# Performance work log

Measured on AMD Instinct MI355X. Metric: run time of the kernel, lower is better.

Reference implementation:

```python
import jax, jax.numpy as jnp
import numpy as np

T, B, D = 32, 16, 128


def _evolve(xr, xi, U):
    # xr, xi: [T,B,D,D]; U: [D,D,2] -> complex U x U^H per matrix
    Ur, Ui = U[..., 0], U[..., 1]
    r = jnp.einsum('ij,tbjk->tbik', Ur, xr) - jnp.einsum('ij,tbjk->tbik', Ui, xi)
    i = jnp.einsum('ij,tbjk->tbik', Ui, xr) + jnp.einsum('ij,tbjk->tbik', Ur, xi)
    out_r = jnp.einsum('tbik,jk->tbij', r, Ur) + jnp.einsum('tbik,jk->tbij', i, Ui)
    out_i = jnp.einsum('tbik,jk->tbij', i, Ur) - jnp.einsum('tbik,jk->tbij', r, Ui)
    return out_r, out_i


def _forward(inputs_real, inputs_imag, Uq, Uk, Uv):
    qr, qi = _evolve(inputs_real, inputs_imag, Uq)
    kr, ki = _evolve(inputs_real, inputs_imag, Uk)
    vr, vi = _evolve(inputs_real, inputs_imag, Uv)
    # trace(A @ B) = sum_ij A_ij * B_ji -> distance scores [Tq, Tk, B]
    tr_r = jnp.einsum('qbij,kbji->qkb', qr, kr) - jnp.einsum('qbij,kbji->qkb', qi, ki)
    tr_i = jnp.einsum('qbij,kbji->qkb', qr, ki) + jnp.einsum('qbij,kbji->qkb', qi, kr)
    dist = jnp.sqrt(tr_r * tr_r + tr_i * tr_i)
    # original builds scores via torch.tensor(list) -> values are detached
    dist = jax.lax.stop_gradient(dist)
    # original applies softmax over the LAST dim of the [Tk, B] score matrix,
    # i.e. over the batch dim (faithful reproduction)
    S = jax.nn.softmax(dist, axis=-1)  # [Tq, Tk, B]
    # original zip(values[0], values[1], scores) iterates the (real, imag)
    # components of the value at t=0 and t=1 against score rows 0 and 1
    s0 = S[:, 0, :, None, None]  # [Tq,B,1,1]
    s1 = S[:, 1, :, None, None]
    out_r = vr[0][None] * s0 + vi[0][None] * s1  # [Tq,B,D,D]
    out_i = vr[1][None] * s0 + vi[1][None] * s1
    return out_r, out_i


def setup_inputs() -> dict:
    key = jax.random.key(0)
    k0, k1, k2, k3, k4 = jax.random.split(key, 5)
    inputs_real = jax.random.normal(k0, (T, B, D, D), dtype=jnp.float32)
    inputs_imag = jax.random.normal(k1, (T, B, D, D), dtype=jnp.float32)
    eye = jnp.stack([jnp.eye(D, dtype=jnp.float32), jnp.zeros((D, D), jnp.float32)], axis=-1)
    Uq = eye + 0.05 * jax.random.normal(k2, (D, D, 2), dtype=jnp.float32)
    Uk = eye + 0.05 * jax.random.normal(k3, (D, D, 2), dtype=jnp.float32)
    Uv = eye + 0.05 * jax.random.normal(k4, (D, D, 2), dtype=jnp.float32)
    return {"inputs_real": inputs_real, "inputs_imag": inputs_imag, "Uq": Uq, "Uk": Uk, "Uv": Uv}


def reference(inputs_real, inputs_imag, Uq, Uk, Uv):
    return _forward(inputs_real, inputs_imag, Uq, Uk, Uv)
```

## Files before the change

### kernel.cpp

```cpp
#include <hip/hip_runtime.h>
#include <math.h>

#define MAT 16384
#define OFF_MC   0
#define OFF_MTC  32768
#define OFF_UVTC 65536
#define OFF_ZSR  2129920
#define OFF_ZSI  (OFF_ZSR + 32*16384)
#define OFF_VR   (OFF_ZSI + 32*16384)
#define OFF_VI   (OFF_VR + 32*16384)
#define OFF_TR   (OFF_VI + 32*16384)
#define OFF_S    (OFF_TR + 2048)

__device__ __forceinline__ float dot4(float4 a, float4 b) {
    return a.x*b.x + a.y*b.y + a.z*b.z + a.w*b.w;
}

__global__ __launch_bounds__(128) void k_M(const float* __restrict__ Uq,
                                           const float* __restrict__ Uk,
                                           const float* __restrict__ Uv,
                                           float* __restrict__ ws) {
    const int i = blockIdx.x;
    const int j = threadIdx.x;
    __shared__ float qr_s[128], qi_s[128];
    qr_s[j] = Uq[(j*128 + i)*2 + 0];
    qi_s[j] = Uq[(j*128 + i)*2 + 1];
    __syncthreads();
    const float2* Uk2 = (const float2*)Uk;
    float mr = 0.f, mi = 0.f;
    #pragma unroll 8
    for (int p = 0; p < 128; ++p) {
        float2 k2 = Uk2[p*128 + j];
        float qr = qr_s[p], qi = qi_s[p];
        mr += qr*k2.x + qi*k2.y;
        mi += qr*k2.y - qi*k2.x;
    }
    ws[OFF_MC  + i*256 + 2*j]     = mr;
    ws[OFF_MC  + i*256 + 2*j + 1] = mi;
    ws[OFF_MTC + j*256 + 2*i]     = mr;
    ws[OFF_MTC + j*256 + 2*i + 1] = mi;
    float2 uv = ((const float2*)Uv)[i*128 + j];
    ws[OFF_UVTC + j*256 + 2*i]     = uv.x;
    ws[OFF_UVTC + j*256 + 2*i + 1] = uv.y;
}

__global__ __launch_bounds__(128) void k_fused(const float* __restrict__ xr,
                                               const float* __restrict__ xi,
                                               const float* __restrict__ Uv,
                                               float* __restrict__ ws) {
    const int bid  = blockIdx.x;
    const int m    = bid & 63;
    const int i0   = (bid >> 6) * 8;
    const int tid  = threadIdx.x;
    const int w    = tid >> 6;
    const int lane = tid & 63;
    const int cg   = lane & 31;
    const int kp   = lane >> 5;

    __shared__ __align__(16) float At[2048];
    __shared__ __align__(16) float Tb[2112];

    {
        const float2* Ap2 = (const float2*)((m < 32) ? (ws + OFF_MC) : Uv);
        #pragma unroll
        for (int rr = 0; rr < 8; ++rr) {
            float2 u = Ap2[(i0 + rr)*128 + tid];
            *(float2*)&At[tid*16 + (rr>>2)*8 + (rr&3)*2] = u;
        }
    }
    __syncthreads();

    float yr[4][4], yi[4][4];
    #pragma unroll
    for (int r = 0; r < 4; ++r)
        #pragma unroll
        for (int c = 0; c < 4; ++c) { yr[r][c] = 0.f; yi[r][c] = 0.f; }

    const float4* Xr4 = (const float4*)(xr + (m & 31)*MAT);
    const float4* Xi4 = (const float4*)(xi + (m & 31)*MAT);

    float4 pR0, pI0, pR1, pI1;
#define LDX(T, R, I) do { int _k = 2*(T) + kp;               \
    R = Xr4[_k*32 + cg]; I = Xi4[_k*32 + cg]; } while (0)

#define CFMA_P1(aLo, aHi, Rv, Iv) do {                                   \
    const float ar_[4] = {aLo.x, aLo.z, aHi.x, aHi.z};                   \
    const float ai_[4] = {aLo.y, aLo.w, aHi.y, aHi.w};                   \
    const float br_[4] = {Rv.x, Rv.y, Rv.z, Rv.w};                       \
    const float bi_[4] = {Iv.x, Iv.y, Iv.z, Iv.w};                       \
    _Pragma("unroll")                                                    \
    for (int r = 0; r < 4; ++r) {                                        \
        _Pragma("unroll")                                                \
        for (int c = 0; c < 4; ++c) {                                    \
            yr[r][c] += ar_[r]*br_[c] - ai_[r]*bi_[c];                   \
            yi[r][c] += ar_[r]*bi_[c] + ai_[r]*br_[c];                   \
        }                                                                \
    } } while (0)

    LDX(0, pR0, pI0);
    LDX(1, pR1, pI1);
    #pragma unroll 1
    for (int t = 0; t < 64; t += 2) {
        {
            int kk = 2*t + kp;
            float4 aLo = *(const float4*)&At[kk*16 + w*8];
            float4 aHi = *(const float4*)&At[kk*16 + w*8 + 4];
            CFMA_P1(aLo, aHi, pR0, pI0);
            int tn = (t+2 > 63) ? 63 : t+2; LDX(tn, pR0, pI0);
        }
        {
            int kk = 2*(t+1) + kp;
            float4 aLo = *(const float4*)&At[kk*16 + w*8];
            float4 aHi = *(const float4*)&At[kk*16 + w*8 + 4];
            CFMA_P1(aLo, aHi, pR1, pI1);
            int tn = (t+3 > 63) ? 63 : t+3; LDX(tn, pR1, pI1);
        }
    }

    #pragma unroll
    for (int r = 0; r < 4; ++r)
        #pragma unroll
        for (int c = 0; c < 4; ++c) {
            yr[r][c] += __shfl_xor(yr[r][c], 32);
            yi[r][c] += __shfl_xor(yi[r][c], 32);
        }
    __syncthreads();
    if (kp == 0) {
        #pragma unroll
        for (int c = 0; c < 4; ++c) {
            int col = 4*cg + c;
            *(float4*)&At[col*16 + w*8]     = make_float4(yr[0][c], yi[0][c], yr[1][c], yi[1][c]);
            *(float4*)&At[col*16 + w*8 + 4] = make_float4(yr[2][c], yi[2][c], yr[3][c], yi[3][c]);
        }
    }
    __syncthreads();

    float zr[4][4], zi[4][4];
    #pragma unroll
    for (int r = 0; r < 4; ++r)
        #pragma unroll
        for (int c = 0; c < 4; ++c) { zr[r][c] = 0.f; zi[r][c] = 0.f; }

    const float4* UT4 = (const float4*)(ws + (m < 32 ? OFF_MTC : OFF_UVTC));

    float4 pE0, pO0, pE1, pO1;
#define LDU(T, E, O) do { int _k = 2*(T) + kp;               \
    E = UT4[_k*64 + 2*cg]; O = UT4[_k*64 + 2*cg + 1]; } while (0)

#define CFMA_P2(aLo, aHi, Ev, Ov) do {                                   \
    const float ya_[4] = {aLo.x, aLo.z, aHi.x, aHi.z};                   \
    const float yb_[4] = {aLo.y, aLo.w, aHi.y, aHi.w};                   \
    _Pragma("unroll")                                                    \
    for (int r = 0; r < 4; ++r) {                                        \
        const float yrv = ya_[r], yiv = yb_[r];                          \
        zr[r][0] += yrv*Ev.x + yiv*Ev.y;  zi[r][0] += yiv*Ev.x - yrv*Ev.y; \
        zr[r][1] += yrv*Ev.z + yiv*Ev.w;  zi[r][1] += yiv*Ev.z - yrv*Ev.w; \
        zr[r][2] += yrv*Ov.x + yiv*Ov.y;  zi[r][2] += yiv*Ov.x - yrv*Ov.y; \
        zr[r][3] += yrv*Ov.z + yiv*Ov.w;  zi[r][3] += yiv*Ov.z - yrv*Ov.w; \
    } } while (0)

    LDU(0, pE0, pO0);
    LDU(1, pE1, pO1);
    #pragma unroll 1
    for (int t = 0; t < 64; t += 2) {
        {
            int kk = 2*t + kp;
            float4 aLo = *(const float4*)&At[kk*16 + w*8];
            float4 aHi = *(const float4*)&At[kk*16 + w*8 + 4];
            CFMA_P2(aLo, aHi, pE0, pO0);
            int tn = (t+2 > 63) ? 63 : t+2; LDU(tn, pE0, pO0);
        }
        {
            int kk = 2*(t+1) + kp;
            float4 aLo = *(const float4*)&At[kk*16 + w*8];
            float4 aHi = *(const float4*)&At[kk*16 + w*8 + 4];
            CFMA_P2(aLo, aHi, pE1, pO1);
            int tn = (t+3 > 63) ? 63 : t+3; LDU(tn, pE1, pO1);
        }
    }

    #pragma unroll
    for (int r = 0; r < 4; ++r)
        #pragma unroll
        for (int c = 0; c < 4; ++c) {
            zr[r][c] += __shfl_xor(zr[r][c], 32);
            zi[r][c] += __shfl_xor(zi[r][c], 32);
        }

    if (m < 32) {
        float* T_r = Tb;
        float* T_i = Tb + 1056;
        if (kp == 0) {
            #pragma unroll
            for (int r = 0; r < 4; ++r) {
                int ii = w*4 + r;
                *(float4*)&T_r[ii*132 + 4*cg] = make_float4(zr[r][0], zr[r][1], zr[r][2], zr[r][3]);
                *(float4*)&T_i[ii*132 + 4*cg] = make_float4(zi[r][0], zi[r][1], zi[r][2], zi[r][3]);
            }
        }
        __syncthreads();
        float* dstR = ws + OFF_ZSR + m*MAT;
        float* dstI = ws + OFF_ZSI + m*MAT;
        #pragma unroll
        for (int wl = 0; wl < 8; ++wl) {
            int o  = wl*128 + tid;
            int c  = o >> 3;
            int ii = o & 7;
            dstR[c*128 + i0 + ii] = T_r[ii*132 + c];
            dstI[c*128 + i0 + ii] = T_i[ii*132 + c];
        }
    } else {
        if (kp == 0) {
            float* dstR = ws + OFF_VR + (m-32)*MAT;
            float* dstI = ws + OFF_VI + (m-32)*MAT;
            #pragma unroll
            for (int r = 0; r < 4; ++r) {
                int row = i0 + w*4 + r;
                *(float4*)&dstR[row*128 + 4*cg] = make_float4(zr[r][0], zr[r][1], zr[r][2], zr[r][3]);
                *(float4*)&dstI[row*128 + 4*cg] = make_float4(zi[r][0], zi[r][1], zi[r][2], zi[r][3]);
            }
        }
    }
#undef LDX
#undef LDU
#undef CFMA_P1
#undef CFMA_P2
}

__global__ __launch_bounds__(256) void k_trace(const float* __restrict__ xr,
                                               const float* __restrict__ xi,
                                               float* __restrict__ ws) {
    const int q = blockIdx.x >> 4, b = blockIdx.x & 15;
    const int tid = threadIdx.x;
    const float4* Xr4  = (const float4*)(xr + (q*16 + b)*MAT);
    const float4* Xi4  = (const float4*)(xi + (q*16 + b)*MAT);
    const float4* Z0r4 = (const float4*)(ws + OFF_ZSR + b*MAT);
    const float4* Z0i4 = (const float4*)(ws + OFF_ZSI + b*MAT);
    const float4* Z1r4 = (const float4*)(ws + OFF_ZSR + (16+b)*MAT);
    const float4* Z1i4 = (const float4*)(ws + OFF_ZSI + (16+b)*MAT);
    float r0 = 0.f, s0 = 0.f, r1 = 0.f, s1 = 0.f;
    #pragma unroll 4
    for (int w = 0; w < 16; ++w) {
        int e = w*256 + tid;
        float4 xrv = Xr4[e], xiv = Xi4[e];
        float4 z0r = Z0r4[e], z0i = Z0i4[e];
        float4 z1r = Z1r4[e], z1i = Z1i4[e];
        r0 += dot4(xrv, z0r) - dot4(xiv, z0i);
        s0 += dot4(xrv, z0i) + dot4(xiv, z0r);
        r1 += dot4(xrv, z1r) - dot4(xiv, z1i);
        s1 += dot4(xrv, z1i) + dot4(xiv, z1r);
    }
    #pragma unroll
    for (int off = 32; off > 0; off >>= 1) {
        r0 += __shfl_down(r0, off);
        s0 += __shfl_down(s0, off);
        r1 += __shfl_down(r1, off);
        s1 += __shfl_down(s1, off);
    }
    __shared__ float red[4][4];
    if ((tid & 63) == 0) {
        int wv = tid >> 6;
        red[wv][0] = r0; red[wv][1] = s0; red[wv][2] = r1; red[wv][3] = s1;
    }
    __syncthreads();
    if (tid == 0) {
        float a0 = red[0][0]+red[1][0]+red[2][0]+red[3][0];
        float a1 = red[0][1]+red[1][1]+red[2][1]+red[3][1];
        float a2 = red[0][2]+red[1][2]+red[2][2]+red[3][2];
        float a3 = red[0][3]+red[1][3]+red[2][3]+red[3][3];
        float* trp = ws + OFF_TR;
        trp[((q*2+0)*16 + b)*2 + 0] = a0;
        trp[((q*2+0)*16 + b)*2 + 1] = a1;
        trp[((q*2+1)*16 + b)*2 + 0] = a2;
        trp[((q*2+1)*16 + b)*2 + 1] = a3;
    }
}

__global__ __launch_bounds__(64) void k_softmax(float* __restrict__ ws) {
    const int t = threadIdx.x;
    const float* trp = ws + OFF_TR + t*32;
    float d[16];
    float mx = -1e30f;
    #pragma unroll
    for (int b = 0; b < 16; ++b) {
        float rr = trp[b*2+0], ii = trp[b*2+1];
        d[b] = sqrtf(rr*rr + ii*ii);
        mx = fmaxf(mx, d[b]);
    }
    float sum = 0.f;
    #pragma unroll
    for (int b = 0; b < 16; ++b) { d[b] = expf(d[b] - mx); sum += d[b]; }
    float inv = 1.f / sum;
    #pragma unroll
    for (int b = 0; b < 16; ++b) ws[OFF_S + t*16 + b] = d[b] * inv;
}

__global__ __launch_bounds__(256) void k_out(const float* __restrict__ ws,
                                             float* __restrict__ out) {
    const int t = blockIdx.x >> 4, b = blockIdx.x & 15;
    const float s0 = ws[OFF_S + (t*2+0)*16 + b];
    const float s1 = ws[OFF_S + (t*2+1)*16 + b];
    const float4* Vr0 = (const float4*)(ws + OFF_VR + b*MAT);
    const float4* Vi0 = (const float4*)(ws + OFF_VI + b*MAT);
    const float4* Vr1 = (const float4*)(ws + OFF_VR + (16+b)*MAT);
    const float4* Vi1 = (const float4*)(ws + OFF_VI + (16+b)*MAT);
    float4* outR = (float4*)out + (t*16 + b)*4096;
    float4* outI = (float4*)out + 2097152 + (t*16 + b)*4096;
    #pragma unroll 4
    for (int w = 0; w < 16; ++w) {
        int e = w*256 + threadIdx.x;
        float4 a = Vr0[e], bb = Vi0[e], c = Vr1[e], dd = Vi1[e];
        outR[e] = make_float4(a.x*s0 + bb.x*s1, a.y*s0 + bb.y*s1,
                              a.z*s0 + bb.z*s1, a.w*s0 + bb.w*s1);
        outI[e] = make_float4(c.x*s0 + dd.x*s1, c.y*s0 + dd.y*s1,
                              c.z*s0 + dd.z*s1, c.w*s0 + dd.w*s1);
    }
}

extern "C" void kernel_launch(void* const* d_in, const int* in_sizes, int n_in,
                              void* d_out, int out_size, void* d_ws, size_t ws_size,
                              hipStream_t stream) {
    const float* xr = (const float*)d_in[0];
    const float* xi = (const float*)d_in[1];
    const float* Uq = (const float*)d_in[2];
    const float* Uk = (const float*)d_in[3];
    const float* Uv = (const float*)d_in[4];
    float* ws  = (float*)d_ws;
    float* out = (float*)d_out;

    k_M<<<128, 128, 0, stream>>>(Uq, Uk, Uv, ws);
    k_fused<<<1024, 128, 0, stream>>>(xr, xi, Uv, ws);
    k_trace<<<512, 256, 0, stream>>>(xr, xi, ws);
    k_softmax<<<1, 64, 0, stream>>>(ws);
    k_out<<<512, 256, 0, stream>>>(ws, out);
}
```

Baseline: 97.07 us.

## Fuse softmax into output kernel and software-pipeline shared-memory operand loads

```diff
diff --git a/kernel.cpp b/kernel.cpp
--- a/kernel.cpp
+++ b/kernel.cpp
@@ -10,7 +10,6 @@
 #define OFF_VR   (OFF_ZSI + 32*16384)
 #define OFF_VI   (OFF_VR + 32*16384)
 #define OFF_TR   (OFF_VI + 32*16384)
-#define OFF_S    (OFF_TR + 2048)
 
 __device__ __forceinline__ float dot4(float4 a, float4 b) {
     return a.x*b.x + a.y*b.y + a.z*b.z + a.w*b.w;
@@ -70,6 +69,8 @@
     }
     __syncthreads();
 
+    const float4* At4c = (const float4*)At;
+
     float yr[4][4], yi[4][4];
     #pragma unroll
     for (int r = 0; r < 4; ++r)
@@ -79,9 +80,10 @@
     const float4* Xr4 = (const float4*)(xr + (m & 31)*MAT);
     const float4* Xi4 = (const float4*)(xi + (m & 31)*MAT);
 
-    float4 pR0, pI0, pR1, pI1;
 #define LDX(T, R, I) do { int _k = 2*(T) + kp;               \
     R = Xr4[_k*32 + cg]; I = Xi4[_k*32 + cg]; } while (0)
+#define LDA(T, L, H) do { int _k = 2*(T) + kp;               \
+    L = At4c[_k*4 + w*2]; H = At4c[_k*4 + w*2 + 1]; } while (0)
 
 #define CFMA_P1(aLo, aHi, Rv, Iv) do {                                   \
     const float ar_[4] = {aLo.x, aLo.z, aHi.x, aHi.z};                   \
@@ -97,24 +99,30 @@
         }                                                                \
     } } while (0)
 
-    LDX(0, pR0, pI0);
-    LDX(1, pR1, pI1);
-    #pragma unroll 1
-    for (int t = 0; t < 64; t += 2) {
-        {
-            int kk = 2*t + kp;
-            float4 aLo = *(const float4*)&At[kk*16 + w*8];
-            float4 aHi = *(const float4*)&At[kk*16 + w*8 + 4];
-            CFMA_P1(aLo, aHi, pR0, pI0);
-            int tn = (t+2 > 63) ? 63 : t+2; LDX(tn, pR0, pI0);
-        }
-        {
-            int kk = 2*(t+1) + kp;
-            float4 aLo = *(const float4*)&At[kk*16 + w*8];
-            float4 aHi = *(const float4*)&At[kk*16 + w*8 + 4];
-            CFMA_P1(aLo, aHi, pR1, pI1);
-            int tn = (t+3 > 63) ? 63 : t+3; LDX(tn, pR1, pI1);
-        }
+#define BODY1(CL, CH, BR, BI, TN) do {                       \
+    CFMA_P1(CL, CH, BR, BI);                                 \
+    LDX(TN, BR, BI);                                         \
+    LDA(TN, CL, CH); } while (0)
+
+    {
+        float4 b0R, b0I, b1R, b1I, c0L, c0H, c1L, c1H;
+        LDX(0, b0R, b0I); LDX(1, b1R, b1I);
+        LDA(0, c0L, c0H); LDA(1, c1L, c1H);
+        #pragma unroll 1
+        for (int t = 0; t < 56; t += 4) {
+            BODY1(c0L, c0H, b0R, b0I, t+2);
+            BODY1(c1L, c1H, b1R, b1I, t+3);
+            BODY1(c0L, c0H, b0R, b0I, t+4);
+            BODY1(c1L, c1H, b1R, b1I, t+5);
+        }
+        BODY1(c0L, c0H, b0R, b0I, 58);
+        BODY1(c1L, c1H, b1R, b1I, 59);
+        BODY1(c0L, c0H, b0R, b0I, 60);
+        BODY1(c1L, c1H, b1R, b1I, 61);
+        BODY1(c0L, c0H, b0R, b0I, 62);
+        BODY1(c1L, c1H, b1R, b1I, 63);
+        BODY1(c0L, c0H, b0R, b0I, 63);
+        BODY1(c1L, c1H, b1R, b1I, 63);
     }
 
     #pragma unroll
@@ -143,7 +151,6 @@
 
     const float4* UT4 = (const float4*)(ws + (m < 32 ? OFF_MTC : OFF_UVTC));
 
-    float4 pE0, pO0, pE1, pO1;
 #define LDU(T, E, O) do { int _k = 2*(T) + kp;               \
     E = UT4[_k*64 + 2*cg]; O = UT4[_k*64 + 2*cg + 1]; } while (0)
 
@@ -159,24 +166,30 @@
         zr[r][3] += yrv*Ov.z + yiv*Ov.w;  zi[r][3] += yiv*Ov.z - yrv*Ov.w; \
     } } while (0)
 
-    LDU(0, pE0, pO0);
-    LDU(1, pE1, pO1);
-    #pragma unroll 1
-    for (int t = 0; t < 64; t += 2) {
-        {
-            int kk = 2*t + kp;
-            float4 aLo = *(const float4*)&At[kk*16 + w*8];
-            float4 aHi = *(const float4*)&At[kk*16 + w*8 + 4];
-            CFMA_P2(aLo, aHi, pE0, pO0);
-            int tn = (t+2 > 63) ? 63 : t+2; LDU(tn, pE0, pO0);
-        }
-        {
-            int kk = 2*(t+1) + kp;
-            float4 aLo = *(const float4*)&At[kk*16 + w*8];
-            float4 aHi = *(const float4*)&At[kk*16 + w*8 + 4];
-            CFMA_P2(aLo, aHi, pE1, pO1);
-            int tn = (t+3 > 63) ? 63 : t+3; LDU(tn, pE1, pO1);
-        }
+#define BODY2(CL, CH, BE, BO, TN) do {                       \
+    CFMA_P2(CL, CH, BE, BO);                                 \
+    LDU(TN, BE, BO);                                         \
+    LDA(TN, CL, CH); } while (0)
+
+    {
+        float4 e0, o0, e1, o1, c0L, c0H, c1L, c1H;
+        LDU(0, e0, o0); LDU(1, e1, o1);
+        LDA(0, c0L, c0H); LDA(1, c1L, c1H);
+        #pragma unroll 1
+        for (int t = 0; t < 56; t += 4) {
+            BODY2(c0L, c0H, e0, o0, t+2);
+            BODY2(c1L, c1H, e1, o1, t+3);
+            BODY2(c0L, c0H, e0, o0, t+4);
+            BODY2(c1L, c1H, e1, o1, t+5);
+        }
+        BODY2(c0L, c0H, e0, o0, 58);
+        BODY2(c1L, c1H, e1, o1, 59);
+        BODY2(c0L, c0H, e0, o0, 60);
+        BODY2(c1L, c1H, e1, o1, 61);
+        BODY2(c0L, c0H, e0, o0, 62);
+        BODY2(c1L, c1H, e1, o1, 63);
+        BODY2(c0L, c0H, e0, o0, 63);
+        BODY2(c1L, c1H, e1, o1, 63);
     }
 
     #pragma unroll
@@ -222,9 +235,12 @@
         }
     }
 #undef LDX
+#undef LDA
 #undef LDU
 #undef CFMA_P1
 #undef CFMA_P2
+#undef BODY1
+#undef BODY2
 }
 
 __global__ __launch_bounds__(256) void k_trace(const float* __restrict__ xr,
@@ -276,30 +292,28 @@
     }
 }
 
-__global__ __launch_bounds__(64) void k_softmax(float* __restrict__ ws) {
-    const int t = threadIdx.x;
-    const float* trp = ws + OFF_TR + t*32;
-    float d[16];
-    float mx = -1e30f;
-    #pragma unroll
-    for (int b = 0; b < 16; ++b) {
-        float rr = trp[b*2+0], ii = trp[b*2+1];
-        d[b] = sqrtf(rr*rr + ii*ii);
-        mx = fmaxf(mx, d[b]);
-    }
-    float sum = 0.f;
-    #pragma unroll
-    for (int b = 0; b < 16; ++b) { d[b] = expf(d[b] - mx); sum += d[b]; }
-    float inv = 1.f / sum;
-    #pragma unroll
-    for (int b = 0; b < 16; ++b) ws[OFF_S + t*16 + b] = d[b] * inv;
-}
-
 __global__ __launch_bounds__(256) void k_out(const float* __restrict__ ws,
                                              float* __restrict__ out) {
     const int t = blockIdx.x >> 4, b = blockIdx.x & 15;
-    const float s0 = ws[OFF_S + (t*2+0)*16 + b];
-    const float s1 = ws[OFF_S + (t*2+1)*16 + b];
+    const float* trp = ws + OFF_TR;
+    float d0[16], d1[16];
+    float mx0 = -1e30f, mx1 = -1e30f;
+    #pragma unroll
+    for (int bb = 0; bb < 16; ++bb) {
+        float ar = trp[((t*2+0)*16 + bb)*2 + 0], ai = trp[((t*2+0)*16 + bb)*2 + 1];
+        float br = trp[((t*2+1)*16 + bb)*2 + 0], bi = trp[((t*2+1)*16 + bb)*2 + 1];
+        d0[bb] = sqrtf(ar*ar + ai*ai); mx0 = fmaxf(mx0, d0[bb]);
+        d1[bb] = sqrtf(br*br + bi*bi); mx1 = fmaxf(mx1, d1[bb]);
+    }
+    float sum0 = 0.f, sum1 = 0.f;
+    #pragma unroll
+    for (int bb = 0; bb < 16; ++bb) {
+        d0[bb] = expf(d0[bb] - mx0); sum0 += d0[bb];
+        d1[bb] = expf(d1[bb] - mx1); sum1 += d1[bb];
+    }
+    const float s0 = d0[b] / sum0;
+    const float s1 = d1[b] / sum1;
+
     const float4* Vr0 = (const float4*)(ws + OFF_VR + b*MAT);
     const float4* Vi0 = (const float4*)(ws + OFF_VI + b*MAT);
     const float4* Vr1 = (const float4*)(ws + OFF_VR + (16+b)*MAT);
@@ -331,6 +345,5 @@
     k_M<<<128, 128, 0, stream>>>(Uq, Uk, Uv, ws);
     k_fused<<<1024, 128, 0, stream>>>(xr, xi, Uv, ws);
     k_trace<<<512, 256, 0, stream>>>(xr, xi, ws);
-    k_softmax<<<1, 64, 0, stream>>>(ws);
     k_out<<<512, 256, 0, stream>>>(ws, out);
 }
```

Result: slower. 112.6 us (+16.0%).
